# Optimization experiments

Measured on AMD Instinct MI355X. Metric: run time of the kernel, lower is better.

The kernel has to match this reference:

```python
import jax, jax.numpy as jnp
import numpy as np

N, R, T = 40000, 2000, 500000   # node_size, rel_size, triple_size
D, DEPTH, PROXY_N = 128, 2, 64  # node_F, depth, proxy rows
DC = D * (DEPTH + 1)            # 384


def _unique_edges(rng, n_rows, n_cols, n_edges):
    # sorted, duplicate-free edge list -> matches torch.sparse coalesce() ordering
    keys = np.unique(rng.integers(0, n_rows * n_cols, size=int(n_edges * 1.05), dtype=np.int64))[:n_edges]
    assert keys.shape[0] == n_edges
    return np.stack([keys // n_cols, keys % n_cols], axis=1)


def _init_emb(key, r, c):
    w = jax.random.normal(key, (r, c), dtype=jnp.float32)
    return w / jnp.maximum(jnp.linalg.norm(w, axis=1, keepdims=True), 1e-12)


def setup_inputs() -> dict:
    rng = np.random.default_rng(0)
    adj = jnp.asarray(_unique_edges(rng, N, N, T))                    # [T,2] (src, dst)
    idx = jnp.stack([jnp.arange(T), jnp.asarray(rng.integers(0, R, T, dtype=np.int64))], axis=1)  # [T,2]
    val = jnp.ones((T,), jnp.float32)
    ent_m = jnp.asarray(_unique_edges(rng, N, N, T))
    rel_m = jnp.asarray(_unique_edges(rng, N, R, T))
    ks = jax.random.split(jax.random.key(0), 12)
    return {
        "ent_emb": _init_emb(ks[0], N, D),
        "rel_emb": _init_emb(ks[1], R, D),
        "e_gate": _init_emb(ks[2], DC, DC),
        "e_proxy": _init_emb(ks[3], PROXY_N, DC),
        "e_bias": _init_emb(ks[4], 1, DC),
        "e_attn": jnp.stack([_init_emb(ks[5], D, 1), _init_emb(ks[6], D, 1)]),
        "r_gate": _init_emb(ks[7], DC, DC),
        "r_proxy": _init_emb(ks[8], PROXY_N, DC),
        "r_bias": _init_emb(ks[9], 1, DC),
        "r_attn": jnp.stack([_init_emb(ks[10], D, 1), _init_emb(ks[11], D, 1)]),
        "val_input": val,
        "adj_input": adj,
        "index_input": idx,
        "ent_matrix": ent_m,
        "rel_matrix": rel_m,
    }


def _l2(x):
    return x / jnp.maximum(jnp.linalg.norm(x, axis=-1, keepdims=True), 1e-12)


def _seg_softmax(v, seg, n):
    m = jax.ops.segment_max(v, seg, num_segments=n)
    e = jnp.exp(v - m[seg])
    s = jax.ops.segment_sum(e, seg, num_segments=n)
    return e / s[seg]


def _adj_agg(edges, emb, n_rows):
    # torch.sparse.softmax over rows of an all-ones adjacency, then sparse @ emb
    rows, cols = edges[:, 0], edges[:, 1]
    w = _seg_softmax(jnp.zeros(edges.shape[0], emb.dtype), rows, n_rows)
    return jax.ops.segment_sum(w[:, None] * emb[cols], rows, num_segments=n_rows)


def _graph_attention(features, rel_emb, edges, sp_idx, sp_val, attn, gate_k, proxy, bias):
    n = features.shape[0]
    t = sp_val.shape[0]
    feats = jnp.tanh(features)
    outs = [feats]
    for l in range(DEPTH):
        # sparse (T,R) @ rel_emb -> per-edge relation embedding, then L2 normalize
        rels_sum = _l2(jax.ops.segment_sum(sp_val[:, None] * rel_emb[sp_idx[:, 1]], sp_idx[:, 0], num_segments=t))
        neighs = feats[edges[:, 1]]                                   # [T,D]
        neighs = neighs - 2.0 * jnp.sum(neighs * rels_sum, axis=1, keepdims=True) * rels_sum  # Householder reflection
        att = _seg_softmax((rels_sum @ attn[l])[:, 0], edges[:, 0], n)  # sparse row softmax
        feats = jnp.tanh(jax.ops.segment_sum(neighs * att[:, None], edges[:, 0], num_segments=n))
        outs.append(feats)
    outputs = jnp.concatenate(outs, axis=1)                           # [N, DC]
    pa = jax.nn.softmax(_l2(outputs) @ _l2(proxy).T, axis=-1)         # [N, 64]
    pf = outputs - pa @ proxy
    gate = jax.nn.sigmoid(pf @ gate_k + bias)
    return gate * outputs + (1.0 - gate) * pf


def reference(ent_emb, rel_emb, e_gate, e_proxy, e_bias, e_attn, r_gate, r_proxy, r_bias, r_attn, val_input, adj_input, index_input, ent_matrix, rel_matrix):
    ent_feature = _adj_agg(ent_matrix, ent_emb, N)                    # [N,D]
    rel_feature = _adj_agg(rel_matrix, rel_emb, N)                    # [N,D]
    out_e = _graph_attention(ent_feature, rel_emb, adj_input, index_input, val_input, e_attn, e_gate, e_proxy, e_bias)
    out_r = _graph_attention(rel_feature, rel_emb, adj_input, index_input, val_input, r_attn, r_gate, r_proxy, r_bias)
    # dropout_rate = 0.0 -> identity
    return jnp.concatenate([out_e, out_r], axis=-1)                   # [N, 2*DC]
```

## Files before the change

kernel.cpp:

```cpp
#include <hip/hip_runtime.h>
#include <hip/hip_fp16.h>


typedef __attribute__((ext_vector_type(4))) float f32x4;
typedef _Float16 h16x2 __attribute__((ext_vector_type(2)));
typedef _Float16 f16x8 __attribute__((ext_vector_type(8)));
typedef float f32x16 __attribute__((ext_vector_type(16)));

__device__ __forceinline__ float wave_sum(float v) {
#pragma unroll
  for (int o = 32; o > 0; o >>= 1) v += __shfl_xor(v, o, 64);
  return v;
}
__device__ __forceinline__ float wave_max(float v) {
#pragma unroll
  for (int o = 32; o > 0; o >>= 1) v = fmaxf(v, __shfl_xor(v, o, 64));
  return v;
}
__device__ __forceinline__ unsigned pkhalf2(float a, float b) {
  __half2 h = __floats2half2_rn(a, b);
  return __builtin_bit_cast(unsigned, h);
}
__device__ __forceinline__ float bcf(unsigned u) {
  return __builtin_bit_cast(float, u);
}
__device__ __forceinline__ unsigned short f2h(float x) {
  return __builtin_bit_cast(unsigned short, (_Float16)x);
}
__device__ __forceinline__ float h2f(unsigned short h) {
  return (float)__builtin_bit_cast(_Float16, h);
}
__device__ __forceinline__ float tanh_fast(float x) {
  float t = __expf(-2.f * fabsf(x));
  float y = (1.f - t) / (1.f + t);
  return copysignf(y, x);
}
__device__ __forceinline__ float fdot2u(unsigned a, unsigned b, float c) {
#if __has_builtin(__builtin_amdgcn_fdot2)
  return __builtin_amdgcn_fdot2(__builtin_bit_cast(h16x2, a),
                                __builtin_bit_cast(h16x2, b), c, false);
#else
  h16x2 x = __builtin_bit_cast(h16x2, a), y = __builtin_bit_cast(h16x2, b);
  return fmaf((float)x.x, (float)y.x, fmaf((float)x.y, (float)y.y, c));
#endif
}
__device__ __forceinline__ float dot8(uint4 a, uint4 b) {
  return fdot2u(a.w, b.w, fdot2u(a.z, b.z, fdot2u(a.y, b.y,
         fdot2u(a.x, b.x, 0.f))));
}

__global__ void rowptr3_kernel(const int* __restrict__ e0,
                               const int* __restrict__ e1,
                               const int* __restrict__ e2, int T, int N,
                               int* __restrict__ p0, int* __restrict__ p1,
                               int* __restrict__ p2) {
  int tid = blockIdx.x * blockDim.x + threadIdx.x;
  int which = tid / (N + 1);
  int r = tid - which * (N + 1);
  if (which >= 3) return;
  const int* E = which == 0 ? e0 : (which == 1 ? e1 : e2);
  int* P = which == 0 ? p0 : (which == 1 ? p1 : p2);
  int lo = 0, hi = T;
  while (lo < hi) {
    int mid = (lo + hi) >> 1;
    if (E[2 * mid] < r) lo = mid + 1; else hi = mid;
  }
  P[r] = lo;
}

__global__ void relprep_kernel(const float* __restrict__ rel_emb,
                               const float* __restrict__ e_attn,
                               const float* __restrict__ r_attn, int R,
                               float4* __restrict__ expS4,
                               unsigned* __restrict__ rnorm,
                               unsigned* __restrict__ rel16) {
  int r = blockIdx.x * 4 + (threadIdx.x >> 6);
  int lane = threadIdx.x & 63;
  if (r >= R) return;
  float2 v  = *(const float2*)(rel_emb + (size_t)r * 128 + 2 * lane);
  float2 a0 = *(const float2*)(e_attn + 2 * lane);
  float2 a1 = *(const float2*)(e_attn + 128 + 2 * lane);
  float2 b0 = *(const float2*)(r_attn + 2 * lane);
  float2 b1 = *(const float2*)(r_attn + 128 + 2 * lane);
  float n  = wave_sum(v.x * v.x + v.y * v.y);
  float d0 = wave_sum(v.x * a0.x + v.y * a0.y);
  float d1 = wave_sum(v.x * a1.x + v.y * a1.y);
  float d2 = wave_sum(v.x * b0.x + v.y * b0.y);
  float d3 = wave_sum(v.x * b1.x + v.y * b1.y);
  float inv = 1.f / fmaxf(sqrtf(n), 1e-12f);
  rnorm[(size_t)r * 64 + lane] = pkhalf2(v.x * inv, v.y * inv);
  rel16[(size_t)r * 64 + lane] = pkhalf2(v.x, v.y);
  if (lane == 0) {
    expS4[r] = make_float4(__expf(d0 * inv), __expf(d1 * inv),
                           __expf(d2 * inv), __expf(d3 * inv));
  }
}

__global__ void pack_f16_kernel(const float* __restrict__ src,
                                unsigned* __restrict__ dst, int n2) {
  int i = blockIdx.x * blockDim.x + threadIdx.x;
  if (i >= n2) return;
  float2 v = *(const float2*)(src + 2 * (size_t)i);
  dst[i] = pkhalf2(v.x, v.y);
}

__global__ void pack_edges_kernel(const int* __restrict__ adj,
                                  const int* __restrict__ idx,
                                  unsigned* __restrict__ pk, int T) {
  int e = blockIdx.x * blockDim.x + threadIdx.x;
  if (e >= T) return;
  pk[e] = (unsigned)adj[2 * e + 1] | ((unsigned)idx[2 * e + 1] << 16);
}

__global__ __launch_bounds__(256) void stats4_kernel(
    const int* __restrict__ ptr, const unsigned* __restrict__ pk,
    const float4* __restrict__ expS4, float4* __restrict__ inv4, int N) {
  int r = blockIdx.x * 4 + (threadIdx.x >> 6);
  if (r >= N) return;
  int lane = threadIdx.x & 63;
  int beg = ptr[r], end = ptr[r + 1];
  float d0 = 0.f, d1 = 0.f, d2 = 0.f, d3 = 0.f;
  for (int e = beg + lane; e < end; e += 64) {
    float4 es = expS4[pk[e] >> 16];
    d0 += es.x; d1 += es.y; d2 += es.z; d3 += es.w;
  }
#pragma unroll
  for (int o = 32; o > 0; o >>= 1) {
    d0 += __shfl_xor(d0, o, 64); d1 += __shfl_xor(d1, o, 64);
    d2 += __shfl_xor(d2, o, 64); d3 += __shfl_xor(d3, o, 64);
  }
  if (lane == 0) {
    inv4[r] = make_float4(d0 > 0.f ? 1.f / d0 : 0.f,
                          d1 > 0.f ? 1.f / d1 : 0.f,
                          d2 > 0.f ? 1.f / d2 : 0.f,
                          d3 > 0.f ? 1.f / d3 : 0.f);
  }
}

__global__ void weight_kernel(const int* __restrict__ adj,
                              const unsigned* __restrict__ pk,
                              const float4* __restrict__ expS4,
                              const float4* __restrict__ inv4,
                              uint2* __restrict__ wt0,
                              uint2* __restrict__ wt1, int T) {
  int e = blockIdx.x * blockDim.x + threadIdx.x;
  if (e >= T) return;
  int row = adj[2 * e];
  int rel = (int)(pk[e] >> 16);
  float4 es = expS4[rel];
  float4 iv = inv4[row];
  wt0[e] = make_uint2(__builtin_bit_cast(unsigned, es.x * iv.x),
                      __builtin_bit_cast(unsigned, es.z * iv.z));
  wt1[e] = make_uint2(__builtin_bit_cast(unsigned, es.y * iv.y),
                      __builtin_bit_cast(unsigned, es.w * iv.w));
}

__global__ __launch_bounds__(256) void agg_fused_kernel(
    const int* __restrict__ ptrE, const int* __restrict__ edgesE,
    const unsigned* __restrict__ ent16, const int* __restrict__ ptrR,
    const int* __restrict__ edgesR, const unsigned* __restrict__ rel16,
    unsigned* __restrict__ fout, int N) {
  int r = blockIdx.x * 4 + (threadIdx.x >> 6);
  if (r >= N) return;
  int lane = threadIdx.x & 63;
  int g = lane >> 4, q = lane & 15;

  float aE[8] = {0, 0, 0, 0, 0, 0, 0, 0};
  float aR[8] = {0, 0, 0, 0, 0, 0, 0, 0};

  auto addh = [&](uint4 u, float* a) {
    h16x2 h0 = __builtin_bit_cast(h16x2, u.x), h1 = __builtin_bit_cast(h16x2, u.y);
    h16x2 h2 = __builtin_bit_cast(h16x2, u.z), h3 = __builtin_bit_cast(h16x2, u.w);
    a[0] += (float)h0.x; a[1] += (float)h0.y;
    a[2] += (float)h1.x; a[3] += (float)h1.y;
    a[4] += (float)h2.x; a[5] += (float)h2.y;
    a[6] += (float)h3.x; a[7] += (float)h3.y;
  };

  int begE = ptrE[r], endE = ptrE[r + 1];
  for (int e0 = begE; e0 < endE; e0 += 8) {
    int eA = e0 + g, eB = e0 + 4 + g;
    if (eA < endE)
      addh(*(const uint4*)(ent16 + (size_t)edgesE[2 * eA + 1] * 64 + 4 * q), aE);
    if (eB < endE)
      addh(*(const uint4*)(ent16 + (size_t)edgesE[2 * eB + 1] * 64 + 4 * q), aE);
  }
  int begR = ptrR[r], endR = ptrR[r + 1];
  for (int e0 = begR; e0 < endR; e0 += 8) {
    int eA = e0 + g, eB = e0 + 4 + g;
    if (eA < endR)
      addh(*(const uint4*)(rel16 + (size_t)edgesR[2 * eA + 1] * 64 + 4 * q), aR);
    if (eB < endR)
      addh(*(const uint4*)(rel16 + (size_t)edgesR[2 * eB + 1] * 64 + 4 * q), aR);
  }
#pragma unroll
  for (int j = 0; j < 8; ++j) {
    aE[j] += __shfl_xor(aE[j], 16, 64); aE[j] += __shfl_xor(aE[j], 32, 64);
    aR[j] += __shfl_xor(aR[j], 16, 64); aR[j] += __shfl_xor(aR[j], 32, 64);
  }
  float sE = (endE > begE) ? 1.f / (float)(endE - begE) : 0.f;
  float sR = (endR > begR) ? 1.f / (float)(endR - begR) : 0.f;
  if (g == 0) {
    float t[8];
#pragma unroll
    for (int j = 0; j < 8; ++j) t[j] = tanh_fast(aE[j] * sE);
    uint4 u;
    u.x = pkhalf2(t[0], t[1]); u.y = pkhalf2(t[2], t[3]);
    u.z = pkhalf2(t[4], t[5]); u.w = pkhalf2(t[6], t[7]);
    *(uint4*)(fout + (size_t)r * 128 + 4 * q) = u;
  } else if (g == 1) {
    float t[8];
#pragma unroll
    for (int j = 0; j < 8; ++j) t[j] = tanh_fast(aR[j] * sR);
    uint4 u;
    u.x = pkhalf2(t[0], t[1]); u.y = pkhalf2(t[2], t[3]);
    u.z = pkhalf2(t[4], t[5]); u.w = pkhalf2(t[6], t[7]);
    *(uint4*)(fout + (size_t)r * 128 + 64 + 4 * q) = u;
  }
}

__global__ __launch_bounds__(256) void layer_rec_kernel(
    const int* __restrict__ ptr, const unsigned* __restrict__ pk,
    const uint2* __restrict__ wt, const unsigned* __restrict__ rnorm,
    const unsigned* __restrict__ fin, unsigned* __restrict__ foutE,
    unsigned* __restrict__ foutR, int fstride, int N) {
  int r = blockIdx.x * 4 + (threadIdx.x >> 6);
  if (r >= N) return;
  int lane = threadIdx.x & 63;
  int g = lane >> 4, q = lane & 15;
  int beg = ptr[r], end = ptr[r + 1];

  float aE[8] = {0, 0, 0, 0, 0, 0, 0, 0};
  float aR[8] = {0, 0, 0, 0, 0, 0, 0, 0};

  auto accum = [&](uint4 F, uint4 V, float w, float s, float* a) {
    h16x2 f0 = __builtin_bit_cast(h16x2, F.x), v0 = __builtin_bit_cast(h16x2, V.x);
    h16x2 f1 = __builtin_bit_cast(h16x2, F.y), v1 = __builtin_bit_cast(h16x2, V.y);
    h16x2 f2 = __builtin_bit_cast(h16x2, F.z), v2 = __builtin_bit_cast(h16x2, V.z);
    h16x2 f3 = __builtin_bit_cast(h16x2, F.w), v3 = __builtin_bit_cast(h16x2, V.w);
    a[0] = fmaf((float)f0.x, w, fmaf((float)v0.x, s, a[0]));
    a[1] = fmaf((float)f0.y, w, fmaf((float)v0.y, s, a[1]));
    a[2] = fmaf((float)f1.x, w, fmaf((float)v1.x, s, a[2]));
    a[3] = fmaf((float)f1.y, w, fmaf((float)v1.y, s, a[3]));
    a[4] = fmaf((float)f2.x, w, fmaf((float)v2.x, s, a[4]));
    a[5] = fmaf((float)f2.y, w, fmaf((float)v2.y, s, a[5]));
    a[6] = fmaf((float)f3.x, w, fmaf((float)v3.x, s, a[6]));
    a[7] = fmaf((float)f3.y, w, fmaf((float)v3.y, s, a[7]));
  };

  for (int e0 = beg; e0 < end; e0 += 8) {
    int eA = e0 + g, eB = e0 + 4 + g;
    bool actA = eA < end, actB = eB < end;
    unsigned pkA = actA ? pk[eA] : 0u;
    unsigned pkB = actB ? pk[eB] : 0u;
    uint2 wA = actA ? wt[eA] : make_uint2(0u, 0u);
    uint2 wB = actB ? wt[eB] : make_uint2(0u, 0u);
    int colA = (int)(pkA & 0xFFFFu), relA = (int)(pkA >> 16);
    int colB = (int)(pkB & 0xFFFFu), relB = (int)(pkB >> 16);
    float wAE = bcf(wA.x), wAR = bcf(wA.y);
    float wBE = bcf(wB.x), wBR = bcf(wB.y);

    const unsigned* fA = fin + (size_t)colA * 128;
    const unsigned* fB = fin + (size_t)colB * 128;
    uint4 EA = *(const uint4*)(fA + 4 * q);
    uint4 RA = *(const uint4*)(fA + 64 + 4 * q);
    uint4 VA = *(const uint4*)(rnorm + (size_t)relA * 64 + 4 * q);
    uint4 EB = *(const uint4*)(fB + 4 * q);
    uint4 RB = *(const uint4*)(fB + 64 + 4 * q);
    uint4 VB = *(const uint4*)(rnorm + (size_t)relB * 64 + 4 * q);

    float dAE = dot8(EA, VA), dAR = dot8(RA, VA);
    float dBE = dot8(EB, VB), dBR = dot8(RB, VB);
#pragma unroll
    for (int m = 1; m < 16; m <<= 1) {
      dAE += __shfl_xor(dAE, m, 64);
      dAR += __shfl_xor(dAR, m, 64);
      dBE += __shfl_xor(dBE, m, 64);
      dBR += __shfl_xor(dBR, m, 64);
    }
    float sAE = -2.f * wAE * dAE, sAR = -2.f * wAR * dAR;
    float sBE = -2.f * wBE * dBE, sBR = -2.f * wBR * dBR;
    accum(EA, VA, wAE, sAE, aE);
    accum(RA, VA, wAR, sAR, aR);
    accum(EB, VB, wBE, sBE, aE);
    accum(RB, VB, wBR, sBR, aR);
  }

#pragma unroll
  for (int j = 0; j < 8; ++j) {
    aE[j] += __shfl_xor(aE[j], 16, 64); aE[j] += __shfl_xor(aE[j], 32, 64);
    aR[j] += __shfl_xor(aR[j], 16, 64); aR[j] += __shfl_xor(aR[j], 32, 64);
  }
  if (g == 0) {
    float t[8];
#pragma unroll
    for (int j = 0; j < 8; ++j) t[j] = tanh_fast(aE[j]);
    uint4 u;
    u.x = pkhalf2(t[0], t[1]); u.y = pkhalf2(t[2], t[3]);
    u.z = pkhalf2(t[4], t[5]); u.w = pkhalf2(t[6], t[7]);
    *(uint4*)(foutE + (size_t)r * fstride + 4 * q) = u;
  } else if (g == 1) {
    float t[8];
#pragma unroll
    for (int j = 0; j < 8; ++j) t[j] = tanh_fast(aR[j]);
    uint4 u;
    u.x = pkhalf2(t[0], t[1]); u.y = pkhalf2(t[2], t[3]);
    u.z = pkhalf2(t[4], t[5]); u.w = pkhalf2(t[6], t[7]);
    *(uint4*)(foutR + (size_t)r * fstride + 4 * q) = u;
  }
}

__device__ __forceinline__ void pack_one32(const float* __restrict__ src,
                                           unsigned short* __restrict__ dst,
                                           int NT, int srcld, int mode, int f,
                                           int lane) {
  int kt = f / NT, nt = f % NT;
  int kbase = 16 * kt + 8 * (lane >> 5);
  int n = 32 * nt + (lane & 31);
  unsigned short tmp[8];
#pragma unroll
  for (int j = 0; j < 8; ++j) {
    int k = kbase + j;
    float v = (mode == 0) ? src[(size_t)k * srcld + n] : src[(size_t)n * srcld + k];
    tmp[j] = f2h(v);
  }
  *(uint4*)(dst + ((size_t)f * 64 + lane) * 8) = *(uint4*)tmp;
}
__global__ void pack_all_kernel(const float* eP, const float* eG,
                                const float* rP, const float* rG,
                                unsigned short* b1e, unsigned short* b2e,
                                unsigned short* b3e, unsigned short* b1r,
                                unsigned short* b2r, unsigned short* b3r) {
  int f = blockIdx.x * 4 + (threadIdx.x >> 6);
  int lane = threadIdx.x & 63;
  if (f < 48)       pack_one32(eP, b1e, 2, 384, 1, f, lane);
  else if (f < 96)  pack_one32(eP, b2e, 12, 384, 0, f - 48, lane);
  else if (f < 384) pack_one32(eG, b3e, 12, 384, 0, f - 96, lane);
  else if (f < 432) pack_one32(rP, b1r, 2, 384, 1, f - 384, lane);
  else if (f < 480) pack_one32(rP, b2r, 12, 384, 0, f - 432, lane);
  else if (f < 768) pack_one32(rG, b3r, 12, 384, 0, f - 480, lane);
}

__global__ __launch_bounds__(256) void final_fused_kernel(
    const unsigned* __restrict__ f0, const unsigned* __restrict__ f1,
    const unsigned* __restrict__ outu,
    const unsigned short* __restrict__ B1e, const unsigned short* __restrict__ B2e,
    const unsigned short* __restrict__ B3e, const unsigned short* __restrict__ B1r,
    const unsigned short* __restrict__ B2r, const unsigned short* __restrict__ B3r,
    const float* __restrict__ biasE, const float* __restrict__ biasR,
    float* __restrict__ gout) {
  __shared__ __align__(16) unsigned sOutH[32][204];
  __shared__ __align__(16) float sPa[32][68];
  __shared__ __align__(16) unsigned short sPaH[32][72];
  __shared__ float sInv[32];
  unsigned short* sOutHs = (unsigned short*)&sOutH[0][0];

  const int side = blockIdx.x & 1;
  const int row0 = (blockIdx.x >> 1) * 32;
  const int plane = side ? 64 : 0;
  const unsigned* f2 = outu + (side ? 704 : 0);
  const unsigned short* B1 = side ? B1r : B1e;
  const unsigned short* B2 = side ? B2r : B2e;
  const unsigned short* B3 = side ? B3r : B3e;
  const float* bias = side ? biasR : biasE;
  const int coloff = side ? 384 : 0;

  const int t = threadIdx.x;
  const int w = t >> 6, lane = t & 63;
  const int l31 = lane & 31, l5 = lane >> 5;

  {
    int rloc = t >> 3;
    int c0 = t & 7;
    int rg = row0 + rloc;
    float ss = 0.f;
#pragma unroll
    for (int i = 0; i < 6; ++i) {
      int c = c0 + 8 * i;
      int buf = c >> 4, j = c & 15;
      const unsigned* src;
      if (buf == 0)      src = f0 + (size_t)rg * 128 + plane + 4 * j;
      else if (buf == 1) src = f1 + (size_t)rg * 128 + plane + 4 * j;
      else               src = f2 + (size_t)rg * 768 + 4 * j;
      uint4 u = *(const uint4*)src;
      *(uint4*)&sOutH[rloc][c * 4] = u;
      ss = fdot2u(u.x, u.x, fdot2u(u.y, u.y,
           fdot2u(u.z, u.z, fdot2u(u.w, u.w, ss))));
    }
    ss += __shfl_xor(ss, 1, 64);
    ss += __shfl_xor(ss, 2, 64);
    ss += __shfl_xor(ss, 4, 64);
    if (c0 == 0) sInv[rloc] = 1.f / fmaxf(sqrtf(ss), 1e-12f);
  }
  __syncthreads();

  if (w < 2) {
    int ct = w;
    f32x16 acc = {0.f, 0.f, 0.f, 0.f, 0.f, 0.f, 0.f, 0.f,
                  0.f, 0.f, 0.f, 0.f, 0.f, 0.f, 0.f, 0.f};
#pragma unroll
    for (int kt = 0; kt < 24; ++kt) {
      f16x8 a = __builtin_bit_cast(
          f16x8, *(const uint4*)&sOutH[l31][8 * kt + 4 * l5]);
      f16x8 b = *(const f16x8*)(B1 + ((size_t)(kt * 2 + ct) * 64 + lane) * 8);
      acc = __builtin_amdgcn_mfma_f32_32x32x16_f16(a, b, acc, 0, 0, 0);
    }
#pragma unroll
    for (int reg = 0; reg < 16; ++reg) {
      int row = (reg & 3) + 8 * (reg >> 2) + 4 * l5;
      sPa[row][ct * 32 + l31] = acc[reg] * sInv[row];
    }
  }
  __syncthreads();

  for (int rr = 8 * w; rr < 8 * w + 8; ++rr) {
    float v = sPa[rr][lane];
    float mx = wave_max(v);
    float e = __expf(v - mx);
    float s = wave_sum(e);
    sPaH[rr][lane] = f2h(e / s);
  }
  __syncthreads();

  const int ntb = 3 * w;
  unsigned outv[3][8];
  {
    f32x16 acc2[3];
#pragma unroll
    for (int s = 0; s < 3; ++s)
#pragma unroll
      for (int i = 0; i < 16; ++i) acc2[s][i] = 0.f;
#pragma unroll
    for (int kt = 0; kt < 4; ++kt) {
      f16x8 a = __builtin_bit_cast(
          f16x8, *(const uint4*)&sPaH[l31][16 * kt + 8 * l5]);
#pragma unroll
      for (int s = 0; s < 3; ++s) {
        f16x8 b = *(const f16x8*)(B2 + ((size_t)(kt * 12 + ntb + s) * 64 + lane) * 8);
        acc2[s] = __builtin_amdgcn_mfma_f32_32x32x16_f16(a, b, acc2[s], 0, 0, 0);
      }
    }
#pragma unroll
    for (int s = 0; s < 3; ++s) {
      int col = 32 * (ntb + s) + l31;
#pragma unroll
      for (int p = 0; p < 8; ++p) {
        int ra = ((2 * p) & 3) + 8 * (p >> 1) + 4 * l5;
        unsigned short u0 = sOutHs[ra * 408 + col];
        unsigned short u1 = sOutHs[(ra + 1) * 408 + col];
        outv[s][p] = (unsigned)u0 | ((unsigned)u1 << 16);
        float pf0 = h2f(u0) - acc2[s][2 * p];
        float pf1 = h2f(u1) - acc2[s][2 * p + 1];
        sOutHs[ra * 408 + col] = f2h(pf0);
        sOutHs[(ra + 1) * 408 + col] = f2h(pf1);
      }
    }
  }
  __syncthreads();

  f32x16 acc3[3];
#pragma unroll
  for (int s = 0; s < 3; ++s)
#pragma unroll
    for (int i = 0; i < 16; ++i) acc3[s][i] = 0.f;
#pragma unroll
  for (int kt = 0; kt < 24; ++kt) {
    f16x8 a = __builtin_bit_cast(
        f16x8, *(const uint4*)&sOutH[l31][8 * kt + 4 * l5]);
#pragma unroll
    for (int s = 0; s < 3; ++s) {
      f16x8 b = *(const f16x8*)(B3 + ((size_t)(kt * 12 + ntb + s) * 64 + lane) * 8);
      acc3[s] = __builtin_amdgcn_mfma_f32_32x32x16_f16(a, b, acc3[s], 0, 0, 0);
    }
  }

#pragma unroll
  for (int s = 0; s < 3; ++s) {
    int col = 32 * (ntb + s) + l31;
    float bv = bias[col];
#pragma unroll
    for (int p = 0; p < 8; ++p) {
      int ra = ((2 * p) & 3) + 8 * (p >> 1) + 4 * l5;
      float g0 = 1.f / (1.f + __expf(-(acc3[s][2 * p] + bv)));
      float g1 = 1.f / (1.f + __expf(-(acc3[s][2 * p + 1] + bv)));
      float pf0 = h2f(sOutHs[ra * 408 + col]);
      float pf1 = h2f(sOutHs[(ra + 1) * 408 + col]);
      unsigned ov = outv[s][p];
      float o0 = h2f((unsigned short)(ov & 0xffffu));
      float o1 = h2f((unsigned short)(ov >> 16));
      gout[(size_t)(row0 + ra) * 768 + coloff + col] = g0 * o0 + (1.f - g0) * pf0;
      gout[(size_t)(row0 + ra + 1) * 768 + coloff + col] =
          g1 * o1 + (1.f - g1) * pf1;
    }
  }
}

extern "C" void kernel_launch(void* const* d_in, const int* in_sizes, int n_in,
                              void* d_out, int out_size, void* d_ws,
                              size_t ws_size, hipStream_t stream) {
  (void)n_in; (void)out_size; (void)ws_size;
  const float* ent_emb = (const float*)d_in[0];
  const float* rel_emb = (const float*)d_in[1];
  const float* e_gate  = (const float*)d_in[2];
  const float* e_proxy = (const float*)d_in[3];
  const float* e_bias  = (const float*)d_in[4];
  const float* e_attn  = (const float*)d_in[5];
  const float* r_gate  = (const float*)d_in[6];
  const float* r_proxy = (const float*)d_in[7];
  const float* r_bias  = (const float*)d_in[8];
  const float* r_attn  = (const float*)d_in[9];
  const int* adj   = (const int*)d_in[11];
  const int* idx   = (const int*)d_in[12];
  const int* ent_m = (const int*)d_in[13];
  const int* rel_m = (const int*)d_in[14];
  const int N = in_sizes[0] / 128;
  const int R = in_sizes[1] / 128;
  const int T = in_sizes[10];
  float* out = (float*)d_out;

  char* w = (char*)d_ws;
  size_t used = 0;
  auto alloc = [&](size_t bytes) {
    void* p = (void*)(w + used);
    used += (bytes + 255) & ~(size_t)255;
    return p;
  };
  int* ptr_adj  = (int*)alloc((size_t)(N + 1) * sizeof(int));
  int* ptr_ent  = (int*)alloc((size_t)(N + 1) * sizeof(int));
  int* ptr_rel  = (int*)alloc((size_t)(N + 1) * sizeof(int));
  unsigned short* b1e = (unsigned short*)alloc(48 * 1024);
  unsigned short* b2e = (unsigned short*)alloc(48 * 1024);
  unsigned short* b3e = (unsigned short*)alloc(288 * 1024);
  unsigned short* b1r = (unsigned short*)alloc(48 * 1024);
  unsigned short* b2r = (unsigned short*)alloc(48 * 1024);
  unsigned short* b3r = (unsigned short*)alloc(288 * 1024);
  unsigned* rnorm = (unsigned*)alloc((size_t)R * 64 * 4);
  unsigned* rel16 = (unsigned*)alloc((size_t)R * 64 * 4);
  unsigned* ent16 = (unsigned*)alloc((size_t)N * 64 * 4);
  unsigned* fsrc0 = (unsigned*)alloc((size_t)N * 128 * 4);
  unsigned* fsrc1 = (unsigned*)alloc((size_t)N * 128 * 4);
  float4* expS4 = (float4*)alloc((size_t)R * 16);
  float4* inv4  = (float4*)alloc((size_t)N * 16);
  unsigned* pk = (unsigned*)alloc((size_t)T * 4);
  uint2* wt0 = (uint2*)alloc((size_t)T * 8);
  uint2* wt1 = (uint2*)alloc((size_t)T * 8);

  dim3 b256(256);
  rowptr3_kernel<<<(3 * (N + 1) + 255) / 256, b256, 0, stream>>>(
      adj, ent_m, rel_m, T, N, ptr_adj, ptr_ent, ptr_rel);
  relprep_kernel<<<(R + 3) / 4, b256, 0, stream>>>(rel_emb, e_attn, r_attn, R,
                                                   expS4, rnorm, rel16);
  pack_f16_kernel<<<(N * 64 + 255) / 256, b256, 0, stream>>>(ent_emb, ent16,
                                                             N * 64);
  pack_edges_kernel<<<(T + 255) / 256, b256, 0, stream>>>(adj, idx, pk, T);
  pack_all_kernel<<<192, b256, 0, stream>>>(e_proxy, e_gate, r_proxy, r_gate,
                                            b1e, b2e, b3e, b1r, b2r, b3r);

  int grow = (N + 3) / 4;
  stats4_kernel<<<grow, b256, 0, stream>>>(ptr_adj, pk, expS4, inv4, N);
  weight_kernel<<<(T + 255) / 256, b256, 0, stream>>>(adj, pk, expS4, inv4,
                                                      wt0, wt1, T);
  agg_fused_kernel<<<grow, b256, 0, stream>>>(ptr_ent, ent_m, ent16, ptr_rel,
                                              rel_m, rel16, fsrc0, N);
  unsigned* outu = (unsigned*)out;
  layer_rec_kernel<<<grow, b256, 0, stream>>>(ptr_adj, pk, wt0, rnorm, fsrc0,
                                              fsrc1, fsrc1 + 64, 128, N);
  layer_rec_kernel<<<grow, b256, 0, stream>>>(ptr_adj, pk, wt1, rnorm, fsrc1,
                                              outu, outu + 704, 768, N);

  int fblocks = 2 * ((N + 31) / 32);
  final_fused_kernel<<<fblocks, b256, 0, stream>>>(
      fsrc0, fsrc1, outu, b1e, b2e, b3e, b1r, b2r, b3r, e_bias, r_bias, out);
}
```

Before: 282.9 us.

## Merge prep kernels into one launch and fuse stats, weights and aggregation

Measured after the change: 292.7 us. +3.4%, slower.

```diff
diff --git a/kernel.cpp b/kernel.cpp
--- a/kernel.cpp
+++ b/kernel.cpp
@@ -49,12 +49,11 @@
          fdot2u(a.x, b.x, 0.f))));
 }
 
-__global__ void rowptr3_kernel(const int* __restrict__ e0,
-                               const int* __restrict__ e1,
-                               const int* __restrict__ e2, int T, int N,
-                               int* __restrict__ p0, int* __restrict__ p1,
-                               int* __restrict__ p2) {
-  int tid = blockIdx.x * blockDim.x + threadIdx.x;
+__device__ void rowptr_part(int tid, const int* __restrict__ e0,
+                            const int* __restrict__ e1,
+                            const int* __restrict__ e2, int T, int N,
+                            int* __restrict__ p0, int* __restrict__ p1,
+                            int* __restrict__ p2) {
   int which = tid / (N + 1);
   int r = tid - which * (N + 1);
   if (which >= 3) return;
@@ -68,13 +67,13 @@
   P[r] = lo;
 }
 
-__global__ void relprep_kernel(const float* __restrict__ rel_emb,
-                               const float* __restrict__ e_attn,
-                               const float* __restrict__ r_attn, int R,
-                               float4* __restrict__ expS4,
-                               unsigned* __restrict__ rnorm,
-                               unsigned* __restrict__ rel16) {
-  int r = blockIdx.x * 4 + (threadIdx.x >> 6);
+__device__ void relprep_part(int bi, const float* __restrict__ rel_emb,
+                             const float* __restrict__ e_attn,
+                             const float* __restrict__ r_attn, int R,
+                             float4* __restrict__ expS4,
+                             unsigned* __restrict__ rnorm,
+                             unsigned* __restrict__ rel16) {
+  int r = bi * 4 + (threadIdx.x >> 6);
   int lane = threadIdx.x & 63;
   if (r >= R) return;
   float2 v  = *(const float2*)(rel_emb + (size_t)r * 128 + 2 * lane);
@@ -96,26 +95,80 @@
   }
 }
 
-__global__ void pack_f16_kernel(const float* __restrict__ src,
-                                unsigned* __restrict__ dst, int n2) {
-  int i = blockIdx.x * blockDim.x + threadIdx.x;
+__device__ void pack_f16_part(int i, const float* __restrict__ src,
+                              unsigned* __restrict__ dst, int n2) {
   if (i >= n2) return;
   float2 v = *(const float2*)(src + 2 * (size_t)i);
   dst[i] = pkhalf2(v.x, v.y);
 }
 
-__global__ void pack_edges_kernel(const int* __restrict__ adj,
-                                  const int* __restrict__ idx,
-                                  unsigned* __restrict__ pk, int T) {
-  int e = blockIdx.x * blockDim.x + threadIdx.x;
+__device__ void pack_edges_part(int e, const int* __restrict__ adj,
+                                const int* __restrict__ idx,
+                                unsigned* __restrict__ pk, int T) {
   if (e >= T) return;
   pk[e] = (unsigned)adj[2 * e + 1] | ((unsigned)idx[2 * e + 1] << 16);
 }
 
-__global__ __launch_bounds__(256) void stats4_kernel(
-    const int* __restrict__ ptr, const unsigned* __restrict__ pk,
-    const float4* __restrict__ expS4, float4* __restrict__ inv4, int N) {
-  int r = blockIdx.x * 4 + (threadIdx.x >> 6);
+__device__ __forceinline__ void pack_one32(const float* __restrict__ src,
+                                           unsigned short* __restrict__ dst,
+                                           int NT, int srcld, int mode, int f,
+                                           int lane) {
+  int kt = f / NT, nt = f % NT;
+  int kbase = 16 * kt + 8 * (lane >> 5);
+  int n = 32 * nt + (lane & 31);
+  unsigned short tmp[8];
+#pragma unroll
+  for (int j = 0; j < 8; ++j) {
+    int k = kbase + j;
+    float v = (mode == 0) ? src[(size_t)k * srcld + n] : src[(size_t)n * srcld + k];
+    tmp[j] = f2h(v);
+  }
+  *(uint4*)(dst + ((size_t)f * 64 + lane) * 8) = *(uint4*)tmp;
+}
+__device__ void pack_all_part(int bi, const float* eP, const float* eG,
+                              const float* rP, const float* rG,
+                              unsigned short* b1e, unsigned short* b2e,
+                              unsigned short* b3e, unsigned short* b1r,
+                              unsigned short* b2r, unsigned short* b3r) {
+  int f = bi * 4 + (threadIdx.x >> 6);
+  int lane = threadIdx.x & 63;
+  if (f < 48)       pack_one32(eP, b1e, 2, 384, 1, f, lane);
+  else if (f < 96)  pack_one32(eP, b2e, 12, 384, 0, f - 48, lane);
+  else if (f < 384) pack_one32(eG, b3e, 12, 384, 0, f - 96, lane);
+  else if (f < 432) pack_one32(rP, b1r, 2, 384, 1, f - 384, lane);
+  else if (f < 480) pack_one32(rP, b2r, 12, 384, 0, f - 432, lane);
+  else if (f < 768) pack_one32(rG, b3r, 12, 384, 0, f - 480, lane);
+}
+
+__global__ __launch_bounds__(256) void prep_uber_kernel(
+    const int* adj, const int* idx, const int* ent_m, const int* rel_m, int T,
+    int N, int* p0, int* p1, int* p2, const float* rel_emb,
+    const float* e_attn, const float* r_attn, int R, float4* expS4,
+    unsigned* rnorm, unsigned* rel16, const float* ent_emb, unsigned* ent16,
+    unsigned* pk, const float* eP, const float* eG, const float* rP,
+    const float* rG, unsigned short* b1e, unsigned short* b2e,
+    unsigned short* b3e, unsigned short* b1r, unsigned short* b2r,
+    unsigned short* b3r, int o1, int o2, int o3, int o4) {
+  int b = blockIdx.x;
+  if (b < o1) {
+    rowptr_part(b * 256 + threadIdx.x, adj, ent_m, rel_m, T, N, p0, p1, p2);
+  } else if (b < o2) {
+    relprep_part(b - o1, rel_emb, e_attn, r_attn, R, expS4, rnorm, rel16);
+  } else if (b < o3) {
+    pack_f16_part((b - o2) * 256 + threadIdx.x, ent_emb, ent16, N * 64);
+  } else if (b < o4) {
+    pack_edges_part((b - o3) * 256 + threadIdx.x, adj, idx, pk, T);
+  } else {
+    pack_all_part(b - o4, eP, eG, rP, rG, b1e, b2e, b3e, b1r, b2r, b3r);
+  }
+}
+
+__device__ void stats4w_part(int bi, const int* __restrict__ ptr,
+                             const unsigned* __restrict__ pk,
+                             const float4* __restrict__ expS4,
+                             uint2* __restrict__ wt0, uint2* __restrict__ wt1,
+                             int N) {
+  int r = bi * 4 + (threadIdx.x >> 6);
   if (r >= N) return;
   int lane = threadIdx.x & 63;
   int beg = ptr[r], end = ptr[r + 1];
@@ -129,38 +182,27 @@
     d0 += __shfl_xor(d0, o, 64); d1 += __shfl_xor(d1, o, 64);
     d2 += __shfl_xor(d2, o, 64); d3 += __shfl_xor(d3, o, 64);
   }
-  if (lane == 0) {
-    inv4[r] = make_float4(d0 > 0.f ? 1.f / d0 : 0.f,
-                          d1 > 0.f ? 1.f / d1 : 0.f,
-                          d2 > 0.f ? 1.f / d2 : 0.f,
-                          d3 > 0.f ? 1.f / d3 : 0.f);
-  }
-}
-
-__global__ void weight_kernel(const int* __restrict__ adj,
-                              const unsigned* __restrict__ pk,
-                              const float4* __restrict__ expS4,
-                              const float4* __restrict__ inv4,
-                              uint2* __restrict__ wt0,
-                              uint2* __restrict__ wt1, int T) {
-  int e = blockIdx.x * blockDim.x + threadIdx.x;
-  if (e >= T) return;
-  int row = adj[2 * e];
-  int rel = (int)(pk[e] >> 16);
-  float4 es = expS4[rel];
-  float4 iv = inv4[row];
-  wt0[e] = make_uint2(__builtin_bit_cast(unsigned, es.x * iv.x),
-                      __builtin_bit_cast(unsigned, es.z * iv.z));
-  wt1[e] = make_uint2(__builtin_bit_cast(unsigned, es.y * iv.y),
-                      __builtin_bit_cast(unsigned, es.w * iv.w));
-}
-
-__global__ __launch_bounds__(256) void agg_fused_kernel(
-    const int* __restrict__ ptrE, const int* __restrict__ edgesE,
-    const unsigned* __restrict__ ent16, const int* __restrict__ ptrR,
-    const int* __restrict__ edgesR, const unsigned* __restrict__ rel16,
-    unsigned* __restrict__ fout, int N) {
-  int r = blockIdx.x * 4 + (threadIdx.x >> 6);
+  float i0 = d0 > 0.f ? 1.f / d0 : 0.f;
+  float i1 = d1 > 0.f ? 1.f / d1 : 0.f;
+  float i2 = d2 > 0.f ? 1.f / d2 : 0.f;
+  float i3 = d3 > 0.f ? 1.f / d3 : 0.f;
+  for (int e = beg + lane; e < end; e += 64) {
+    float4 es = expS4[pk[e] >> 16];
+    wt0[e] = make_uint2(__builtin_bit_cast(unsigned, es.x * i0),
+                        __builtin_bit_cast(unsigned, es.z * i2));
+    wt1[e] = make_uint2(__builtin_bit_cast(unsigned, es.y * i1),
+                        __builtin_bit_cast(unsigned, es.w * i3));
+  }
+}
+
+__device__ void agg_part(int bi, const int* __restrict__ ptrE,
+                         const int* __restrict__ edgesE,
+                         const unsigned* __restrict__ ent16,
+                         const int* __restrict__ ptrR,
+                         const int* __restrict__ edgesR,
+                         const unsigned* __restrict__ rel16,
+                         unsigned* __restrict__ fout, int N) {
+  int r = bi * 4 + (threadIdx.x >> 6);
   if (r >= N) return;
   int lane = threadIdx.x & 63;
   int g = lane >> 4, q = lane & 15;
@@ -216,6 +258,19 @@
     u.x = pkhalf2(t[0], t[1]); u.y = pkhalf2(t[2], t[3]);
     u.z = pkhalf2(t[4], t[5]); u.w = pkhalf2(t[6], t[7]);
     *(uint4*)(fout + (size_t)r * 128 + 64 + 4 * q) = u;
+  }
+}
+
+__global__ __launch_bounds__(256) void statsagg_kernel(
+    const int* ptr_adj, const unsigned* pk, const float4* expS4, uint2* wt0,
+    uint2* wt1, const int* ptrE, const int* edgesE, const unsigned* ent16,
+    const int* ptrR, const int* edgesR, const unsigned* rel16, unsigned* fout,
+    int N) {
+  int bi = blockIdx.x >> 1;
+  if (blockIdx.x & 1) {
+    agg_part(bi, ptrE, edgesE, ent16, ptrR, edgesR, rel16, fout, N);
+  } else {
+    stats4w_part(bi, ptr_adj, pk, expS4, wt0, wt1, N);
   }
 }
 
@@ -308,37 +363,6 @@
     u.z = pkhalf2(t[4], t[5]); u.w = pkhalf2(t[6], t[7]);
     *(uint4*)(foutR + (size_t)r * fstride + 4 * q) = u;
   }
-}
-
-__device__ __forceinline__ void pack_one32(const float* __restrict__ src,
-                                           unsigned short* __restrict__ dst,
-                                           int NT, int srcld, int mode, int f,
-                                           int lane) {
-  int kt = f / NT, nt = f % NT;
-  int kbase = 16 * kt + 8 * (lane >> 5);
-  int n = 32 * nt + (lane & 31);
-  unsigned short tmp[8];
-#pragma unroll
-  for (int j = 0; j < 8; ++j) {
-    int k = kbase + j;
-    float v = (mode == 0) ? src[(size_t)k * srcld + n] : src[(size_t)n * srcld + k];
-    tmp[j] = f2h(v);
-  }
-  *(uint4*)(dst + ((size_t)f * 64 + lane) * 8) = *(uint4*)tmp;
-}
-__global__ void pack_all_kernel(const float* eP, const float* eG,
-                                const float* rP, const float* rG,
-                                unsigned short* b1e, unsigned short* b2e,
-                                unsigned short* b3e, unsigned short* b1r,
-                                unsigned short* b2r, unsigned short* b3r) {
-  int f = blockIdx.x * 4 + (threadIdx.x >> 6);
-  int lane = threadIdx.x & 63;
-  if (f < 48)       pack_one32(eP, b1e, 2, 384, 1, f, lane);
-  else if (f < 96)  pack_one32(eP, b2e, 12, 384, 0, f - 48, lane);
-  else if (f < 384) pack_one32(eG, b3e, 12, 384, 0, f - 96, lane);
-  else if (f < 432) pack_one32(rP, b1r, 2, 384, 1, f - 384, lane);
-  else if (f < 480) pack_one32(rP, b2r, 12, 384, 0, f - 432, lane);
-  else if (f < 768) pack_one32(rG, b3r, 12, 384, 0, f - 480, lane);
 }
 
 __global__ __launch_bounds__(256) void final_fused_kernel(
@@ -540,28 +564,28 @@
   unsigned* fsrc0 = (unsigned*)alloc((size_t)N * 128 * 4);
   unsigned* fsrc1 = (unsigned*)alloc((size_t)N * 128 * 4);
   float4* expS4 = (float4*)alloc((size_t)R * 16);
-  float4* inv4  = (float4*)alloc((size_t)N * 16);
   unsigned* pk = (unsigned*)alloc((size_t)T * 4);
   uint2* wt0 = (uint2*)alloc((size_t)T * 8);
   uint2* wt1 = (uint2*)alloc((size_t)T * 8);
 
   dim3 b256(256);
-  rowptr3_kernel<<<(3 * (N + 1) + 255) / 256, b256, 0, stream>>>(
-      adj, ent_m, rel_m, T, N, ptr_adj, ptr_ent, ptr_rel);
-  relprep_kernel<<<(R + 3) / 4, b256, 0, stream>>>(rel_emb, e_attn, r_attn, R,
-                                                   expS4, rnorm, rel16);
-  pack_f16_kernel<<<(N * 64 + 255) / 256, b256, 0, stream>>>(ent_emb, ent16,
-                                                             N * 64);
-  pack_edges_kernel<<<(T + 255) / 256, b256, 0, stream>>>(adj, idx, pk, T);
-  pack_all_kernel<<<192, b256, 0, stream>>>(e_proxy, e_gate, r_proxy, r_gate,
-                                            b1e, b2e, b3e, b1r, b2r, b3r);
+  int nb0 = (3 * (N + 1) + 255) / 256;
+  int nb1 = (R + 3) / 4;
+  int nb2 = (N * 64 + 255) / 256;
+  int nb3 = (T + 255) / 256;
+  int nb4 = 192;
+  int o1 = nb0, o2 = o1 + nb1, o3 = o2 + nb2, o4 = o3 + nb3;
+  int prep_blocks = o4 + nb4;
+  prep_uber_kernel<<<prep_blocks, b256, 0, stream>>>(
+      adj, idx, ent_m, rel_m, T, N, ptr_adj, ptr_ent, ptr_rel, rel_emb,
+      e_attn, r_attn, R, expS4, rnorm, rel16, ent_emb, ent16, pk, e_proxy,
+      e_gate, r_proxy, r_gate, b1e, b2e, b3e, b1r, b2r, b3r, o1, o2, o3, o4);
 
   int grow = (N + 3) / 4;
-  stats4_kernel<<<grow, b256, 0, stream>>>(ptr_adj, pk, expS4, inv4, N);
-  weight_kernel<<<(T + 255) / 256, b256, 0, stream>>>(adj, pk, expS4, inv4,
-                                                      wt0, wt1, T);
-  agg_fused_kernel<<<grow, b256, 0, stream>>>(ptr_ent, ent_m, ent16, ptr_rel,
-                                              rel_m, rel16, fsrc0, N);
+  statsagg_kernel<<<2 * grow, b256, 0, stream>>>(
+      ptr_adj, pk, expS4, wt0, wt1, ptr_ent, ent_m, ent16, ptr_rel, rel_m,
+      rel16, fsrc0, N);
+
   unsigned* outu = (unsigned*)out;
   layer_rec_kernel<<<grow, b256, 0, stream>>>(ptr_adj, pk, wt0, rnorm, fsrc0,
                                               fsrc1, fsrc1 + 64, 128, N);
```
